# Kernel optimization log

Measured on AMD Instinct MI355X. Metric: run time of the kernel, lower is better.

The kernel has to match this reference:

```python
import jax, jax.numpy as jnp
import numpy as np

EPS = 1e-5

def conv1x1_bn(x, W, b, gamma, beta, mean, var):
    # x: (B,C,H,W); W: (O,C) 1x1 conv; BN in eval mode with running stats
    y = jnp.einsum('bchw,oc->bohw', x, W) + b[None, :, None, None]
    scale = gamma / jnp.sqrt(var + EPS)
    return y * scale[None, :, None, None] + (beta - mean * scale)[None, :, None, None]

def setup_inputs() -> dict:
    key = jax.random.key(0)
    ks = jax.random.split(key, 12)
    B, C, H, W = 8, 64, 128, 256
    d = {
        'fea_left': jax.random.normal(ks[0], (B, C, H, W), jnp.float32),
        'fea_right': jax.random.normal(ks[1], (B, C, H, W), jnp.float32),
        'Wq': jax.random.normal(ks[2], (C, C), jnp.float32) * (1.0 / np.sqrt(C)),
        'bq': jax.random.normal(ks[3], (C,), jnp.float32) * 0.02,
        'gq': 1.0 + 0.1 * jax.random.normal(ks[4], (C,), jnp.float32),
        'betaq': 0.02 * jax.random.normal(ks[5], (C,), jnp.float32),
        'mq': 0.02 * jax.random.normal(ks[6], (C,), jnp.float32),
        'vq': jax.random.uniform(ks[7], (C,), jnp.float32, 0.5, 1.5),
        'Wk': jax.random.normal(ks[8], (C, C), jnp.float32) * (1.0 / np.sqrt(C)),
        'bk': jax.random.normal(ks[9], (C,), jnp.float32) * 0.02,
        'gk': 1.0 + 0.1 * jax.random.normal(ks[10], (C,), jnp.float32),
        'betak': 0.02 * jax.random.normal(ks[11], (C,), jnp.float32),
        'mk': 0.02 * jax.random.normal(jax.random.fold_in(key, 100), (C,), jnp.float32),
        'vk': jax.random.uniform(jax.random.fold_in(key, 101), (C,), jnp.float32, 0.5, 1.5),
    }
    return d

def _attend(src, tgt, Wq, bq, gq, betaq, mq, vq, Wk, bk, gk, betak, mk, vk):
    # query from src, key from tgt, values are raw tgt features
    c = src.shape[1]
    Q = conv1x1_bn(src, Wq, bq, gq, betaq, mq, vq)   # (B,C,H,W)
    K = conv1x1_bn(tgt, Wk, bk, gk, betak, mk, vk)   # (B,C,H,W)
    # cost: (B,H,Wq,Wk) = Q^T K over channels, per image row
    cost = jnp.einsum('bchw,bchv->bhwv', Q, K) / c
    attn = jax.nn.softmax(cost, axis=-1)
    out = jnp.einsum('bhwv,bchv->bchw', attn, tgt)   # back to (B,C,H,W)
    return out

def reference(fea_left, fea_right, Wq, bq, gq, betaq, mq, vq, Wk, bk, gk, betak, mk, vk):
    cxr = _attend(fea_left, fea_right, Wq, bq, gq, betaq, mq, vq, Wk, bk, gk, betak, mk, vk)
    enh = _attend(fea_right, fea_left, Wq, bq, gq, betaq, mq, vq, Wk, bk, gk, betak, mk, vk)
    return (cxr, enh)
```

## Files before the change

### kernel.cpp

```cpp
#include <hip/hip_runtime.h>

#define HW_ 32768
#define OUTHALF 16777216ULL
#define SMEM_BYTES 117760

typedef short short8  __attribute__((ext_vector_type(8)));
typedef short short4v __attribute__((ext_vector_type(4)));
typedef float f32x4   __attribute__((ext_vector_type(4)));

__device__ __forceinline__ unsigned short f2bf(float f) {
  unsigned u = __builtin_bit_cast(unsigned, f);
  u += 0x7fffu + ((u >> 16) & 1u);
  return (unsigned short)(u >> 16);
}
__device__ __forceinline__ float bf2f(short s) {
  unsigned u = ((unsigned)(unsigned short)s) << 16;
  return __builtin_bit_cast(float, u);
}
__device__ __forceinline__ char* swz(char* base, int row, int colByte) {
  return base + row * 128 + (colByte ^ ((row & 7) << 4));
}
__device__ __forceinline__ f32x4 zero4() { f32x4 z = {0.f, 0.f, 0.f, 0.f}; return z; }

__global__ void pam_setup(const float* __restrict__ Wq, const float* __restrict__ bq,
                          const float* __restrict__ gq, const float* __restrict__ betaq,
                          const float* __restrict__ mq, const float* __restrict__ vq,
                          const float* __restrict__ Wk, const float* __restrict__ gk,
                          const float* __restrict__ vk,
                          short* __restrict__ Mb, float* __restrict__ u) {
  int blk = blockIdx.x, tid = threadIdx.x;
  if (blk < 16) {
    int entry = blk * 256 + tid;
    int x = entry >> 6, y = entry & 63;
    float acc = 0.f;
    for (int o = 0; o < 64; ++o) {
      float sq = gq[o] * rsqrtf(vq[o] + 1e-5f);
      float sk = gk[o] * rsqrtf(vk[o] + 1e-5f);
      acc += Wq[o * 64 + x] * sq * Wk[o * 64 + y] * sk;
    }
    Mb[x * 64 + y] = (short)f2bf(acc);
  } else if (tid < 64) {
    int y = tid;
    float acc = 0.f;
    for (int o = 0; o < 64; ++o) {
      float sq = gq[o] * rsqrtf(vq[o] + 1e-5f);
      float sk = gk[o] * rsqrtf(vk[o] + 1e-5f);
      float bqq = bq[o] * sq + betaq[o] - mq[o] * sq;
      acc += bqq * Wk[o * 64 + y] * sk;
    }
    u[y] = acc;
  }
}

__global__ __launch_bounds__(512, 2) void pam_main(
    const float* __restrict__ fl, const float* __restrict__ fr,
    const short* __restrict__ Mb, const float* __restrict__ uvec,
    float* __restrict__ out) {
  extern __shared__ __align__(16) char sm[];
  char* XLt = sm;
  char* XRt = sm + 32768;
  char* Kt  = sm + 65536;
  char* Xn  = sm + 73728;
  char* Pt  = sm + 81920;
  float* tl = (float*)(sm + 114688);
  float* Db = (float*)(sm + 116736);

  const int tid  = threadIdx.x;
  const int lane = tid & 63;
  const int wave = tid >> 6;
  const int l15  = lane & 15;
  const int g    = lane >> 4;
  const int bb   = blockIdx.x >> 7;
  const int hh   = blockIdx.x & 127;
  const int rowOff = hh * 256;
  const int base_b = bb * 64;

  for (int it = 0; it < 16; ++it) {
    int unit = it * 512 + tid;
    int tensor = unit >> 12;
    int rem = unit & 4095;
    int cq = rem >> 8;
    int p  = rem & 255;
    const float* src = tensor ? fr : fl;
    char* dst = tensor ? XRt : XLt;
    int gbase = (base_b + cq * 4) * HW_ + rowOff + p;
    float v0 = src[gbase];
    float v1 = src[gbase + HW_];
    float v2 = src[gbase + 2 * HW_];
    float v3 = src[gbase + 3 * HW_];
    short4v pk;
    pk[0] = (short)f2bf(v0); pk[1] = (short)f2bf(v1);
    pk[2] = (short)f2bf(v2); pk[3] = (short)f2bf(v3);
    *(short4v*)swz(dst, p, cq * 8) = pk;
  }
  __syncthreads();

  {
    int sel = tid >> 8;
    int p   = tid & 255;
    char* xt = sel ? XLt : XRt;
    float acc = 0.f;
    #pragma unroll
    for (int j = 0; j < 8; ++j) {
      short8 xv = *(const short8*)swz(xt, p, j * 16);
      #pragma unroll
      for (int e = 0; e < 8; ++e)
        acc = fmaf(bf2f(xv[e]), uvec[j * 8 + e], acc);
    }
    tl[sel * 256 + p] = acc * 0.015625f;
  }

  const short8* mbv = (const short8*)Mb;

  for (int at = 0; at < 2; ++at) {
    char* Xq  = at ? XRt : XLt;
    char* Xkv = at ? XLt : XRt;
    const float* skv = at ? fl : fr;
    const float* tp  = tl + at * 256;
    float* outp = out + (at ? OUTHALF : 0) + (size_t)base_b * HW_ + rowOff;

    f32x4 acc_o[2][4];
    #pragma unroll
    for (int i = 0; i < 2; ++i)
      #pragma unroll
      for (int j = 0; j < 4; ++j) acc_o[i][j] = zero4();
    float dacc0 = 0.f, dacc1 = 0.f;
    const int w0 = wave * 32;

    for (int vt = 0; vt < 4; ++vt) {
      __syncthreads();
      {
        int c  = tid >> 3;
        int v8 = (tid & 7) * 8;
        const float* s = skv + (base_b + c) * HW_ + rowOff + vt * 64 + v8;
        f32x4 A0 = *(const f32x4*)s;
        f32x4 A1 = *(const f32x4*)(s + 4);
        short8 pk;
        pk[0] = (short)f2bf(A0[0]); pk[1] = (short)f2bf(A0[1]);
        pk[2] = (short)f2bf(A0[2]); pk[3] = (short)f2bf(A0[3]);
        pk[4] = (short)f2bf(A1[0]); pk[5] = (short)f2bf(A1[1]);
        pk[6] = (short)f2bf(A1[2]); pk[7] = (short)f2bf(A1[3]);
        *(short8*)swz(Xn, c, v8 * 2) = pk;
      }
      #pragma unroll
      for (int s2 = 0; s2 < 2; ++s2) {
        int sidx = wave * 2 + s2;
        int mi = sidx >> 2, nj = sidx & 3;
        f32x4 accc = zero4();
        #pragma unroll
        for (int kk = 0; kk < 2; ++kk) {
          short8 af = *(const short8*)swz(Xkv, vt * 64 + mi * 16 + l15, (kk * 32 + 8 * g) * 2);
          short8 bf = mbv[(nj * 16 + l15) * 8 + kk * 4 + g];
          accc = __builtin_amdgcn_mfma_f32_16x16x32_bf16(af, bf, accc, 0, 0, 0);
        }
        int e2 = (nj * 16 + l15) * 2;
        #pragma unroll
        for (int r = 0; r < 4; ++r)
          *(short*)swz(Kt, mi * 16 + 4 * g + r, e2) = (short)f2bf(accc[r]);
      }
      __syncthreads();

      short8 bqf[2][2];
      #pragma unroll
      for (int nj = 0; nj < 2; ++nj)
        #pragma unroll
        for (int kk = 0; kk < 2; ++kk)
          bqf[nj][kk] = *(const short8*)swz(Xq, w0 + nj * 16 + l15, (kk * 32 + 8 * g) * 2);

      f32x4 accs[4][2];
      #pragma unroll
      for (int mi = 0; mi < 4; ++mi) {
        accs[mi][0] = zero4(); accs[mi][1] = zero4();
        #pragma unroll
        for (int kk = 0; kk < 2; ++kk) {
          short8 af = *(const short8*)swz(Kt, mi * 16 + l15, (kk * 32 + 8 * g) * 2);
          accs[mi][0] = __builtin_amdgcn_mfma_f32_16x16x32_bf16(af, bqf[0][kk], accs[mi][0], 0, 0, 0);
          accs[mi][1] = __builtin_amdgcn_mfma_f32_16x16x32_bf16(af, bqf[1][kk], accs[mi][1], 0, 0, 0);
        }
      }
      #pragma unroll
      for (int mi = 0; mi < 4; ++mi) {
        f32x4 tr = *(const f32x4*)(tp + vt * 64 + mi * 16 + 4 * g);
        #pragma unroll
        for (int nj = 0; nj < 2; ++nj) {
          f32x4 pv;
          #pragma unroll
          for (int r = 0; r < 4; ++r)
            pv[r] = __expf(fmaf(accs[mi][nj][r], 0.015625f, tr[r]));
          if (nj == 0) dacc0 += pv[0] + pv[1] + pv[2] + pv[3];
          else         dacc1 += pv[0] + pv[1] + pv[2] + pv[3];
          short4v p4;
          p4[0] = (short)f2bf(pv[0]); p4[1] = (short)f2bf(pv[1]);
          p4[2] = (short)f2bf(pv[2]); p4[3] = (short)f2bf(pv[3]);
          *(short4v*)swz(Pt, wave * 32 + nj * 16 + l15, mi * 32 + 8 * g) = p4;
        }
      }
      #pragma unroll
      for (int kk = 0; kk < 2; ++kk) {
        short8 pa0 = *(const short8*)swz(Pt, wave * 32 + l15,      (kk * 32 + 8 * g) * 2);
        short8 pa1 = *(const short8*)swz(Pt, wave * 32 + 16 + l15, (kk * 32 + 8 * g) * 2);
        #pragma unroll
        for (int nj2 = 0; nj2 < 4; ++nj2) {
          short8 xb = *(const short8*)swz(Xn, nj2 * 16 + l15, (kk * 32 + 8 * g) * 2);
          acc_o[0][nj2] = __builtin_amdgcn_mfma_f32_16x16x32_bf16(pa0, xb, acc_o[0][nj2], 0, 0, 0);
          acc_o[1][nj2] = __builtin_amdgcn_mfma_f32_16x16x32_bf16(pa1, xb, acc_o[1][nj2], 0, 0, 0);
        }
      }
    }

    dacc0 += __shfl_xor(dacc0, 16); dacc0 += __shfl_xor(dacc0, 32);
    dacc1 += __shfl_xor(dacc1, 16); dacc1 += __shfl_xor(dacc1, 32);
    if (lane < 16) {
      Db[wave * 32 + lane]      = __builtin_amdgcn_rcpf(dacc0);
      Db[wave * 32 + 16 + lane] = __builtin_amdgcn_rcpf(dacc1);
    }
    #pragma unroll
    for (int mi2 = 0; mi2 < 2; ++mi2) {
      f32x4 rd = *(const f32x4*)(Db + wave * 32 + mi2 * 16 + 4 * g);
      #pragma unroll
      for (int nj2 = 0; nj2 < 4; ++nj2) {
        int c = nj2 * 16 + l15;
        f32x4 v;
        v[0] = acc_o[mi2][nj2][0] * rd[0];
        v[1] = acc_o[mi2][nj2][1] * rd[1];
        v[2] = acc_o[mi2][nj2][2] * rd[2];
        v[3] = acc_o[mi2][nj2][3] * rd[3];
        *(f32x4*)(outp + (size_t)c * HW_ + w0 + mi2 * 16 + 4 * g) = v;
      }
    }
  }
}

extern "C" void kernel_launch(void* const* d_in, const int* in_sizes, int n_in,
                              void* d_out, int out_size, void* d_ws, size_t ws_size,
                              hipStream_t stream) {
  (void)in_sizes; (void)n_in; (void)out_size; (void)ws_size;
  const float* fl    = (const float*)d_in[0];
  const float* fr    = (const float*)d_in[1];
  const float* Wq    = (const float*)d_in[2];
  const float* bq    = (const float*)d_in[3];
  const float* gq    = (const float*)d_in[4];
  const float* betaq = (const float*)d_in[5];
  const float* mq    = (const float*)d_in[6];
  const float* vq    = (const float*)d_in[7];
  const float* Wk    = (const float*)d_in[8];
  const float* gk    = (const float*)d_in[10];
  const float* vk    = (const float*)d_in[13];
  short* Mb = (short*)d_ws;
  float* u  = (float*)((char*)d_ws + 8192);
  float* out = (float*)d_out;

  hipFuncSetAttribute((const void*)pam_main,
                      hipFuncAttributeMaxDynamicSharedMemorySize, SMEM_BYTES);
  pam_setup<<<17, 256, 0, stream>>>(Wq, bq, gq, betaq, mq, vq, Wk, gk, vk, Mb, u);
  pam_main<<<1024, 512, SMEM_BYTES, stream>>>(fl, fr, Mb, u, out);
}
```

Before: 127.3 us.

## Split attention directions across blocks and shrink LDS for higher occupancy

Each block now handles a single attention direction (left→right or right→left) instead of both, which doubles the grid and drops the second transposed tile from shared memory. LDS per block falls from about 115 KB to 66 KB, and launch bounds now allow 4 blocks per CU. Query fragments are loaded straight from global memory into registers, the next value tile is prefetched into registers while the current one is being computed, and the P tile is handled one 16-row half at a time to cut register pressure. In exchange, each row's key/value data is reloaded and reconverted by two blocks, and the strided per-element query loads from global memory may coalesce poorly.

```diff
diff --git a/kernel.cpp b/kernel.cpp
--- a/kernel.cpp
+++ b/kernel.cpp
@@ -2,7 +2,7 @@
 
 #define HW_ 32768
 #define OUTHALF 16777216ULL
-#define SMEM_BYTES 117760
+#define SMEM_BYTES 67584
 
 typedef short short8  __attribute__((ext_vector_type(8)));
 typedef short short4v __attribute__((ext_vector_type(4)));
@@ -52,181 +52,180 @@
   }
 }
 
-__global__ __launch_bounds__(512, 2) void pam_main(
+__global__ __launch_bounds__(512, 4) void pam_main(
     const float* __restrict__ fl, const float* __restrict__ fr,
     const short* __restrict__ Mb, const float* __restrict__ uvec,
     float* __restrict__ out) {
   extern __shared__ __align__(16) char sm[];
-  char* XLt = sm;
-  char* XRt = sm + 32768;
-  char* Kt  = sm + 65536;
-  char* Xn  = sm + 73728;
-  char* Pt  = sm + 81920;
-  float* tl = (float*)(sm + 114688);
-  float* Db = (float*)(sm + 116736);
+  char* Xt = sm;
+  char* Kt = sm + 32768;
+  char* Xn = sm + 40960;
+  char* Pt = sm + 49152;
+  float* tl = (float*)(sm + 65536);
+  float* Db = (float*)(sm + 66560);
 
   const int tid  = threadIdx.x;
   const int lane = tid & 63;
   const int wave = tid >> 6;
   const int l15  = lane & 15;
   const int g    = lane >> 4;
-  const int bb   = blockIdx.x >> 7;
-  const int hh   = blockIdx.x & 127;
+  const int bh   = blockIdx.x >> 1;
+  const int at   = blockIdx.x & 1;
+  const int bb   = bh >> 7;
+  const int hh   = bh & 127;
   const int rowOff = hh * 256;
   const int base_b = bb * 64;
-
-  for (int it = 0; it < 16; ++it) {
+  const int w0   = wave * 32;
+
+  const float* srcq  = at ? fr : fl;
+  const float* srckv = at ? fl : fr;
+  float* outp = out + (at ? OUTHALF : 0) + (size_t)base_b * HW_ + rowOff;
+
+  short8 bqf[2][2];
+  #pragma unroll
+  for (int nj = 0; nj < 2; ++nj) {
+    #pragma unroll
+    for (int kk = 0; kk < 2; ++kk) {
+      const float* qp = srcq + (size_t)(base_b + kk * 32 + 8 * g) * HW_
+                      + rowOff + w0 + nj * 16 + l15;
+      short8 q;
+      #pragma unroll
+      for (int e = 0; e < 8; ++e) q[e] = (short)f2bf(qp[(size_t)e * HW_]);
+      bqf[nj][kk] = q;
+    }
+  }
+
+  #pragma unroll
+  for (int it = 0; it < 8; ++it) {
     int unit = it * 512 + tid;
-    int tensor = unit >> 12;
-    int rem = unit & 4095;
-    int cq = rem >> 8;
-    int p  = rem & 255;
-    const float* src = tensor ? fr : fl;
-    char* dst = tensor ? XRt : XLt;
-    int gbase = (base_b + cq * 4) * HW_ + rowOff + p;
-    float v0 = src[gbase];
-    float v1 = src[gbase + HW_];
-    float v2 = src[gbase + 2 * HW_];
-    float v3 = src[gbase + 3 * HW_];
+    int cq = unit >> 8;
+    int p  = unit & 255;
+    const float* s = srckv + (size_t)(base_b + cq * 4) * HW_ + rowOff + p;
+    float v0 = s[0];
+    float v1 = s[HW_];
+    float v2 = s[2 * HW_];
+    float v3 = s[3 * HW_];
     short4v pk;
     pk[0] = (short)f2bf(v0); pk[1] = (short)f2bf(v1);
     pk[2] = (short)f2bf(v2); pk[3] = (short)f2bf(v3);
-    *(short4v*)swz(dst, p, cq * 8) = pk;
+    *(short4v*)swz(Xt, p, cq * 8) = pk;
   }
   __syncthreads();
 
-  {
-    int sel = tid >> 8;
-    int p   = tid & 255;
-    char* xt = sel ? XLt : XRt;
+  if (tid < 256) {
     float acc = 0.f;
     #pragma unroll
     for (int j = 0; j < 8; ++j) {
-      short8 xv = *(const short8*)swz(xt, p, j * 16);
+      short8 xv = *(const short8*)swz(Xt, tid, j * 16);
       #pragma unroll
       for (int e = 0; e < 8; ++e)
         acc = fmaf(bf2f(xv[e]), uvec[j * 8 + e], acc);
     }
-    tl[sel * 256 + p] = acc * 0.015625f;
+    tl[tid] = acc * 0.015625f;
   }
 
   const short8* mbv = (const short8*)Mb;
-
-  for (int at = 0; at < 2; ++at) {
-    char* Xq  = at ? XRt : XLt;
-    char* Xkv = at ? XLt : XRt;
-    const float* skv = at ? fl : fr;
-    const float* tp  = tl + at * 256;
-    float* outp = out + (at ? OUTHALF : 0) + (size_t)base_b * HW_ + rowOff;
-
-    f32x4 acc_o[2][4];
-    #pragma unroll
-    for (int i = 0; i < 2; ++i)
-      #pragma unroll
-      for (int j = 0; j < 4; ++j) acc_o[i][j] = zero4();
-    float dacc0 = 0.f, dacc1 = 0.f;
-    const int w0 = wave * 32;
-
-    for (int vt = 0; vt < 4; ++vt) {
-      __syncthreads();
-      {
-        int c  = tid >> 3;
-        int v8 = (tid & 7) * 8;
-        const float* s = skv + (base_b + c) * HW_ + rowOff + vt * 64 + v8;
-        f32x4 A0 = *(const f32x4*)s;
-        f32x4 A1 = *(const f32x4*)(s + 4);
-        short8 pk;
-        pk[0] = (short)f2bf(A0[0]); pk[1] = (short)f2bf(A0[1]);
-        pk[2] = (short)f2bf(A0[2]); pk[3] = (short)f2bf(A0[3]);
-        pk[4] = (short)f2bf(A1[0]); pk[5] = (short)f2bf(A1[1]);
-        pk[6] = (short)f2bf(A1[2]); pk[7] = (short)f2bf(A1[3]);
-        *(short8*)swz(Xn, c, v8 * 2) = pk;
+  char* Ptw = Pt + wave * 2048;
+
+  f32x4 acc_o[2][4];
+  #pragma unroll
+  for (int i = 0; i < 2; ++i)
+    #pragma unroll
+    for (int j = 0; j < 4; ++j) acc_o[i][j] = zero4();
+  float dacc0 = 0.f, dacc1 = 0.f;
+
+  const int vc = tid >> 3;
+  const int v8 = (tid & 7) * 8;
+  const float* vbase = srckv + (size_t)(base_b + vc) * HW_ + rowOff + v8;
+  f32x4 A0 = *(const f32x4*)(vbase);
+  f32x4 A1 = *(const f32x4*)(vbase + 4);
+
+  for (int vt = 0; vt < 4; ++vt) {
+    if (vt) __syncthreads();
+    {
+      short8 pk;
+      pk[0] = (short)f2bf(A0[0]); pk[1] = (short)f2bf(A0[1]);
+      pk[2] = (short)f2bf(A0[2]); pk[3] = (short)f2bf(A0[3]);
+      pk[4] = (short)f2bf(A1[0]); pk[5] = (short)f2bf(A1[1]);
+      pk[6] = (short)f2bf(A1[2]); pk[7] = (short)f2bf(A1[3]);
+      *(short8*)swz(Xn, vc, v8 * 2) = pk;
+    }
+    #pragma unroll
+    for (int s2 = 0; s2 < 2; ++s2) {
+      int sidx = wave * 2 + s2;
+      int mi = sidx >> 2, njc = sidx & 3;
+      f32x4 accc = zero4();
+      #pragma unroll
+      for (int kk = 0; kk < 2; ++kk) {
+        short8 af = *(const short8*)swz(Xt, vt * 64 + mi * 16 + l15, (kk * 32 + 8 * g) * 2);
+        short8 bf = mbv[(njc * 16 + l15) * 8 + kk * 4 + g];
+        accc = __builtin_amdgcn_mfma_f32_16x16x32_bf16(af, bf, accc, 0, 0, 0);
       }
-      #pragma unroll
-      for (int s2 = 0; s2 < 2; ++s2) {
-        int sidx = wave * 2 + s2;
-        int mi = sidx >> 2, nj = sidx & 3;
-        f32x4 accc = zero4();
-        #pragma unroll
-        for (int kk = 0; kk < 2; ++kk) {
-          short8 af = *(const short8*)swz(Xkv, vt * 64 + mi * 16 + l15, (kk * 32 + 8 * g) * 2);
-          short8 bf = mbv[(nj * 16 + l15) * 8 + kk * 4 + g];
-          accc = __builtin_amdgcn_mfma_f32_16x16x32_bf16(af, bf, accc, 0, 0, 0);
-        }
-        int e2 = (nj * 16 + l15) * 2;
-        #pragma unroll
-        for (int r = 0; r < 4; ++r)
-          *(short*)swz(Kt, mi * 16 + 4 * g + r, e2) = (short)f2bf(accc[r]);
-      }
-      __syncthreads();
-
-      short8 bqf[2][2];
-      #pragma unroll
-      for (int nj = 0; nj < 2; ++nj)
-        #pragma unroll
-        for (int kk = 0; kk < 2; ++kk)
-          bqf[nj][kk] = *(const short8*)swz(Xq, w0 + nj * 16 + l15, (kk * 32 + 8 * g) * 2);
-
-      f32x4 accs[4][2];
+      int e2 = (njc * 16 + l15) * 2;
+      #pragma unroll
+      for (int r = 0; r < 4; ++r)
+        *(short*)swz(Kt, mi * 16 + 4 * g + r, e2) = (short)f2bf(accc[r]);
+    }
+    __syncthreads();
+
+    if (vt < 3) {
+      A0 = *(const f32x4*)(vbase + (vt + 1) * 64);
+      A1 = *(const f32x4*)(vbase + (vt + 1) * 64 + 4);
+    }
+
+    #pragma unroll
+    for (int nj = 0; nj < 2; ++nj) {
+      float dloc = 0.f;
       #pragma unroll
       for (int mi = 0; mi < 4; ++mi) {
-        accs[mi][0] = zero4(); accs[mi][1] = zero4();
+        f32x4 a = zero4();
         #pragma unroll
         for (int kk = 0; kk < 2; ++kk) {
           short8 af = *(const short8*)swz(Kt, mi * 16 + l15, (kk * 32 + 8 * g) * 2);
-          accs[mi][0] = __builtin_amdgcn_mfma_f32_16x16x32_bf16(af, bqf[0][kk], accs[mi][0], 0, 0, 0);
-          accs[mi][1] = __builtin_amdgcn_mfma_f32_16x16x32_bf16(af, bqf[1][kk], accs[mi][1], 0, 0, 0);
+          a = __builtin_amdgcn_mfma_f32_16x16x32_bf16(af, bqf[nj][kk], a, 0, 0, 0);
         }
+        f32x4 tr = *(const f32x4*)(tl + vt * 64 + mi * 16 + 4 * g);
+        f32x4 pv;
+        #pragma unroll
+        for (int r = 0; r < 4; ++r)
+          pv[r] = __expf(fmaf(a[r], 0.015625f, tr[r]));
+        dloc += pv[0] + pv[1] + pv[2] + pv[3];
+        short4v p4;
+        p4[0] = (short)f2bf(pv[0]); p4[1] = (short)f2bf(pv[1]);
+        p4[2] = (short)f2bf(pv[2]); p4[3] = (short)f2bf(pv[3]);
+        *(short4v*)swz(Ptw, l15, mi * 32 + 8 * g) = p4;
       }
-      #pragma unroll
-      for (int mi = 0; mi < 4; ++mi) {
-        f32x4 tr = *(const f32x4*)(tp + vt * 64 + mi * 16 + 4 * g);
-        #pragma unroll
-        for (int nj = 0; nj < 2; ++nj) {
-          f32x4 pv;
-          #pragma unroll
-          for (int r = 0; r < 4; ++r)
-            pv[r] = __expf(fmaf(accs[mi][nj][r], 0.015625f, tr[r]));
-          if (nj == 0) dacc0 += pv[0] + pv[1] + pv[2] + pv[3];
-          else         dacc1 += pv[0] + pv[1] + pv[2] + pv[3];
-          short4v p4;
-          p4[0] = (short)f2bf(pv[0]); p4[1] = (short)f2bf(pv[1]);
-          p4[2] = (short)f2bf(pv[2]); p4[3] = (short)f2bf(pv[3]);
-          *(short4v*)swz(Pt, wave * 32 + nj * 16 + l15, mi * 32 + 8 * g) = p4;
-        }
-      }
+      if (nj == 0) dacc0 += dloc; else dacc1 += dloc;
       #pragma unroll
       for (int kk = 0; kk < 2; ++kk) {
-        short8 pa0 = *(const short8*)swz(Pt, wave * 32 + l15,      (kk * 32 + 8 * g) * 2);
-        short8 pa1 = *(const short8*)swz(Pt, wave * 32 + 16 + l15, (kk * 32 + 8 * g) * 2);
+        short8 pa = *(const short8*)swz(Ptw, l15, kk * 64 + 16 * g);
         #pragma unroll
         for (int nj2 = 0; nj2 < 4; ++nj2) {
           short8 xb = *(const short8*)swz(Xn, nj2 * 16 + l15, (kk * 32 + 8 * g) * 2);
-          acc_o[0][nj2] = __builtin_amdgcn_mfma_f32_16x16x32_bf16(pa0, xb, acc_o[0][nj2], 0, 0, 0);
-          acc_o[1][nj2] = __builtin_amdgcn_mfma_f32_16x16x32_bf16(pa1, xb, acc_o[1][nj2], 0, 0, 0);
+          acc_o[nj][nj2] = __builtin_amdgcn_mfma_f32_16x16x32_bf16(pa, xb, acc_o[nj][nj2], 0, 0, 0);
         }
       }
     }
-
-    dacc0 += __shfl_xor(dacc0, 16); dacc0 += __shfl_xor(dacc0, 32);
-    dacc1 += __shfl_xor(dacc1, 16); dacc1 += __shfl_xor(dacc1, 32);
-    if (lane < 16) {
-      Db[wave * 32 + lane]      = __builtin_amdgcn_rcpf(dacc0);
-      Db[wave * 32 + 16 + lane] = __builtin_amdgcn_rcpf(dacc1);
-    }
-    #pragma unroll
-    for (int mi2 = 0; mi2 < 2; ++mi2) {
-      f32x4 rd = *(const f32x4*)(Db + wave * 32 + mi2 * 16 + 4 * g);
-      #pragma unroll
-      for (int nj2 = 0; nj2 < 4; ++nj2) {
-        int c = nj2 * 16 + l15;
-        f32x4 v;
-        v[0] = acc_o[mi2][nj2][0] * rd[0];
-        v[1] = acc_o[mi2][nj2][1] * rd[1];
-        v[2] = acc_o[mi2][nj2][2] * rd[2];
-        v[3] = acc_o[mi2][nj2][3] * rd[3];
-        *(f32x4*)(outp + (size_t)c * HW_ + w0 + mi2 * 16 + 4 * g) = v;
-      }
+  }
+
+  dacc0 += __shfl_xor(dacc0, 16); dacc0 += __shfl_xor(dacc0, 32);
+  dacc1 += __shfl_xor(dacc1, 16); dacc1 += __shfl_xor(dacc1, 32);
+  if (lane < 16) {
+    Db[wave * 32 + lane]      = __builtin_amdgcn_rcpf(dacc0);
+    Db[wave * 32 + 16 + lane] = __builtin_amdgcn_rcpf(dacc1);
+  }
+  #pragma unroll
+  for (int mi2 = 0; mi2 < 2; ++mi2) {
+    f32x4 rd = *(const f32x4*)(Db + wave * 32 + mi2 * 16 + 4 * g);
+    #pragma unroll
+    for (int nj2 = 0; nj2 < 4; ++nj2) {
+      int c = nj2 * 16 + l15;
+      f32x4 v;
+      v[0] = acc_o[mi2][nj2][0] * rd[0];
+      v[1] = acc_o[mi2][nj2][1] * rd[1];
+      v[2] = acc_o[mi2][nj2][2] * rd[2];
+      v[3] = acc_o[mi2][nj2][3] * rd[3];
+      *(f32x4*)(outp + (size_t)c * HW_ + w0 + mi2 * 16 + 4 * g) = v;
     }
   }
 }
@@ -253,5 +252,5 @@
   hipFuncSetAttribute((const void*)pam_main,
                       hipFuncAttributeMaxDynamicSharedMemorySize, SMEM_BYTES);
   pam_setup<<<17, 256, 0, stream>>>(Wq, bq, gq, betaq, mq, vq, Wk, gk, vk, Mb, u);
-  pam_main<<<1024, 512, SMEM_BYTES, stream>>>(fl, fr, Mb, u, out);
-}
+  pam_main<<<2048, 512, SMEM_BYTES, stream>>>(fl, fr, Mb, u, out);
+}
```

Result: slower. 164.6 us (+29.3%).

## Project queries through M once per wave and double-buffer value tiles with 1024 threads

Applied to the files above, without the earlier changes.

The blocks grow to 1024 threads, so each of 16 waves owns 16 query columns. Each wave computes its projected query (M^T x_q) once per direction and keeps it in registers, instead of projecting every key tile through M on each iteration. The value tile loads are double-buffered in shared memory with a register prefetch, which leaves one barrier per tile. The risks are register pressure from the launch_bounds(1024,4) request and the occupancy limit set by the roughly 115 KB of shared memory per block.

```diff
diff --git a/kernel.cpp b/kernel.cpp
--- a/kernel.cpp
+++ b/kernel.cpp
@@ -27,18 +27,18 @@
                           const float* __restrict__ mq, const float* __restrict__ vq,
                           const float* __restrict__ Wk, const float* __restrict__ gk,
                           const float* __restrict__ vk,
-                          short* __restrict__ Mb, float* __restrict__ u) {
+                          short* __restrict__ Mbt, float* __restrict__ u) {
   int blk = blockIdx.x, tid = threadIdx.x;
   if (blk < 16) {
     int entry = blk * 256 + tid;
-    int x = entry >> 6, y = entry & 63;
+    int y = entry >> 6, x = entry & 63;
     float acc = 0.f;
     for (int o = 0; o < 64; ++o) {
       float sq = gq[o] * rsqrtf(vq[o] + 1e-5f);
       float sk = gk[o] * rsqrtf(vk[o] + 1e-5f);
       acc += Wq[o * 64 + x] * sq * Wk[o * 64 + y] * sk;
     }
-    Mb[x * 64 + y] = (short)f2bf(acc);
+    Mbt[y * 64 + x] = (short)f2bf(acc);
   } else if (tid < 64) {
     int y = tid;
     float acc = 0.f;
@@ -52,15 +52,14 @@
   }
 }
 
-__global__ __launch_bounds__(512, 2) void pam_main(
+__global__ __launch_bounds__(1024, 4) void pam_main(
     const float* __restrict__ fl, const float* __restrict__ fr,
-    const short* __restrict__ Mb, const float* __restrict__ uvec,
+    const short* __restrict__ Mbt, const float* __restrict__ uvec,
     float* __restrict__ out) {
   extern __shared__ __align__(16) char sm[];
   char* XLt = sm;
   char* XRt = sm + 32768;
-  char* Kt  = sm + 65536;
-  char* Xn  = sm + 73728;
+  char* Xn0 = sm + 65536;
   char* Pt  = sm + 81920;
   float* tl = (float*)(sm + 114688);
   float* Db = (float*)(sm + 116736);
@@ -74,30 +73,28 @@
   const int hh   = blockIdx.x & 127;
   const int rowOff = hh * 256;
   const int base_b = bb * 64;
-
-  for (int it = 0; it < 16; ++it) {
-    int unit = it * 512 + tid;
+  const int w0   = wave * 16;
+
+  char* Ptw = Pt + wave * 2048;
+
+  #pragma unroll
+  for (int it = 0; it < 8; ++it) {
+    int unit = it * 1024 + tid;
     int tensor = unit >> 12;
     int rem = unit & 4095;
     int cq = rem >> 8;
     int p  = rem & 255;
-    const float* src = tensor ? fr : fl;
-    char* dst = tensor ? XRt : XLt;
-    int gbase = (base_b + cq * 4) * HW_ + rowOff + p;
-    float v0 = src[gbase];
-    float v1 = src[gbase + HW_];
-    float v2 = src[gbase + 2 * HW_];
-    float v3 = src[gbase + 3 * HW_];
+    const float* s = (tensor ? fr : fl) + (size_t)(base_b + cq * 4) * HW_ + rowOff + p;
+    float v0 = s[0], v1 = s[HW_], v2 = s[2 * HW_], v3 = s[3 * HW_];
     short4v pk;
     pk[0] = (short)f2bf(v0); pk[1] = (short)f2bf(v1);
     pk[2] = (short)f2bf(v2); pk[3] = (short)f2bf(v3);
-    *(short4v*)swz(dst, p, cq * 8) = pk;
+    *(short4v*)swz(tensor ? XRt : XLt, p, cq * 8) = pk;
   }
   __syncthreads();
 
-  {
-    int sel = tid >> 8;
-    int p   = tid & 255;
+  if (tid < 512) {
+    int sel = tid >> 8, p = tid & 255;
     char* xt = sel ? XLt : XRt;
     float acc = 0.f;
     #pragma unroll
@@ -110,8 +107,7 @@
     tl[sel * 256 + p] = acc * 0.015625f;
   }
 
-  const short8* mbv = (const short8*)Mb;
-
+  #pragma unroll 1
   for (int at = 0; at < 2; ++at) {
     char* Xq  = at ? XRt : XLt;
     char* Xkv = at ? XLt : XRt;
@@ -119,114 +115,106 @@
     const float* tp  = tl + at * 256;
     float* outp = out + (at ? OUTHALF : 0) + (size_t)base_b * HW_ + rowOff;
 
-    f32x4 acc_o[2][4];
+    short8 bq_[2];
+    {
+      short8 xb_[2];
+      #pragma unroll
+      for (int kk = 0; kk < 2; ++kk)
+        xb_[kk] = *(const short8*)swz(Xq, w0 + l15, (kk * 32 + 8 * g) * 2);
+      #pragma unroll
+      for (int mi = 0; mi < 4; ++mi) {
+        f32x4 q = zero4();
+        #pragma unroll
+        for (int kk = 0; kk < 2; ++kk) {
+          short8 am = *(const short8*)(Mbt + (mi * 16 + l15) * 64 + kk * 32 + 8 * g);
+          q = __builtin_amdgcn_mfma_f32_16x16x32_bf16(am, xb_[kk], q, 0, 0, 0);
+        }
+        short4v p4;
+        p4[0] = (short)f2bf(q[0]); p4[1] = (short)f2bf(q[1]);
+        p4[2] = (short)f2bf(q[2]); p4[3] = (short)f2bf(q[3]);
+        *(short4v*)swz(Ptw, l15, mi * 32 + 8 * g) = p4;
+      }
+      #pragma unroll
+      for (int kk = 0; kk < 2; ++kk)
+        bq_[kk] = *(const short8*)swz(Ptw, l15, kk * 64 + 16 * g);
+    }
+
+    f32x4 acc_o[4];
     #pragma unroll
-    for (int i = 0; i < 2; ++i)
-      #pragma unroll
-      for (int j = 0; j < 4; ++j) acc_o[i][j] = zero4();
-    float dacc0 = 0.f, dacc1 = 0.f;
-    const int w0 = wave * 32;
+    for (int j = 0; j < 4; ++j) acc_o[j] = zero4();
+    float dacc = 0.f;
+
+    const int vc = tid >> 4;
+    const int v4 = (tid & 15) * 4;
+    const float* vbase = skv + (size_t)(base_b + vc) * HW_ + rowOff + v4;
+    f32x4 A0 = *(const f32x4*)vbase;
+    {
+      short4v pk;
+      pk[0] = (short)f2bf(A0[0]); pk[1] = (short)f2bf(A0[1]);
+      pk[2] = (short)f2bf(A0[2]); pk[3] = (short)f2bf(A0[3]);
+      *(short4v*)swz(Xn0, vc, v4 * 2) = pk;
+    }
+    A0 = *(const f32x4*)(vbase + 64);
+    __syncthreads();
 
     for (int vt = 0; vt < 4; ++vt) {
-      __syncthreads();
-      {
-        int c  = tid >> 3;
-        int v8 = (tid & 7) * 8;
-        const float* s = skv + (base_b + c) * HW_ + rowOff + vt * 64 + v8;
-        f32x4 A0 = *(const f32x4*)s;
-        f32x4 A1 = *(const f32x4*)(s + 4);
-        short8 pk;
+      if (vt < 3) {
+        short4v pk;
         pk[0] = (short)f2bf(A0[0]); pk[1] = (short)f2bf(A0[1]);
         pk[2] = (short)f2bf(A0[2]); pk[3] = (short)f2bf(A0[3]);
-        pk[4] = (short)f2bf(A1[0]); pk[5] = (short)f2bf(A1[1]);
-        pk[6] = (short)f2bf(A1[2]); pk[7] = (short)f2bf(A1[3]);
-        *(short8*)swz(Xn, c, v8 * 2) = pk;
-      }
-      #pragma unroll
-      for (int s2 = 0; s2 < 2; ++s2) {
-        int sidx = wave * 2 + s2;
-        int mi = sidx >> 2, nj = sidx & 3;
-        f32x4 accc = zero4();
+        *(short4v*)swz(Xn0 + ((vt + 1) & 1) * 8192, vc, v4 * 2) = pk;
+      }
+      if (vt < 2) A0 = *(const f32x4*)(vbase + (vt + 2) * 64);
+      char* XnB = Xn0 + (vt & 1) * 8192;
+
+      f32x4 accs[4];
+      #pragma unroll
+      for (int mi = 0; mi < 4; ++mi) {
+        accs[mi] = zero4();
         #pragma unroll
         for (int kk = 0; kk < 2; ++kk) {
-          short8 af = *(const short8*)swz(Xkv, vt * 64 + mi * 16 + l15, (kk * 32 + 8 * g) * 2);
-          short8 bf = mbv[(nj * 16 + l15) * 8 + kk * 4 + g];
-          accc = __builtin_amdgcn_mfma_f32_16x16x32_bf16(af, bf, accc, 0, 0, 0);
-        }
-        int e2 = (nj * 16 + l15) * 2;
-        #pragma unroll
-        for (int r = 0; r < 4; ++r)
-          *(short*)swz(Kt, mi * 16 + 4 * g + r, e2) = (short)f2bf(accc[r]);
-      }
-      __syncthreads();
-
-      short8 bqf[2][2];
-      #pragma unroll
-      for (int nj = 0; nj < 2; ++nj)
-        #pragma unroll
-        for (int kk = 0; kk < 2; ++kk)
-          bqf[nj][kk] = *(const short8*)swz(Xq, w0 + nj * 16 + l15, (kk * 32 + 8 * g) * 2);
-
-      f32x4 accs[4][2];
-      #pragma unroll
-      for (int mi = 0; mi < 4; ++mi) {
-        accs[mi][0] = zero4(); accs[mi][1] = zero4();
-        #pragma unroll
-        for (int kk = 0; kk < 2; ++kk) {
-          short8 af = *(const short8*)swz(Kt, mi * 16 + l15, (kk * 32 + 8 * g) * 2);
-          accs[mi][0] = __builtin_amdgcn_mfma_f32_16x16x32_bf16(af, bqf[0][kk], accs[mi][0], 0, 0, 0);
-          accs[mi][1] = __builtin_amdgcn_mfma_f32_16x16x32_bf16(af, bqf[1][kk], accs[mi][1], 0, 0, 0);
+          short8 af = *(const short8*)swz(Xkv, vt * 64 + mi * 16 + l15,
+                                          (kk * 32 + 8 * g) * 2);
+          accs[mi] = __builtin_amdgcn_mfma_f32_16x16x32_bf16(af, bq_[kk], accs[mi], 0, 0, 0);
         }
       }
       #pragma unroll
       for (int mi = 0; mi < 4; ++mi) {
         f32x4 tr = *(const f32x4*)(tp + vt * 64 + mi * 16 + 4 * g);
-        #pragma unroll
-        for (int nj = 0; nj < 2; ++nj) {
-          f32x4 pv;
-          #pragma unroll
-          for (int r = 0; r < 4; ++r)
-            pv[r] = __expf(fmaf(accs[mi][nj][r], 0.015625f, tr[r]));
-          if (nj == 0) dacc0 += pv[0] + pv[1] + pv[2] + pv[3];
-          else         dacc1 += pv[0] + pv[1] + pv[2] + pv[3];
-          short4v p4;
-          p4[0] = (short)f2bf(pv[0]); p4[1] = (short)f2bf(pv[1]);
-          p4[2] = (short)f2bf(pv[2]); p4[3] = (short)f2bf(pv[3]);
-          *(short4v*)swz(Pt, wave * 32 + nj * 16 + l15, mi * 32 + 8 * g) = p4;
+        f32x4 pv;
+        #pragma unroll
+        for (int r = 0; r < 4; ++r)
+          pv[r] = __expf(fmaf(accs[mi][r], 0.015625f, tr[r]));
+        dacc += pv[0] + pv[1] + pv[2] + pv[3];
+        short4v p4;
+        p4[0] = (short)f2bf(pv[0]); p4[1] = (short)f2bf(pv[1]);
+        p4[2] = (short)f2bf(pv[2]); p4[3] = (short)f2bf(pv[3]);
+        *(short4v*)swz(Ptw, l15, mi * 32 + 8 * g) = p4;
+      }
+      #pragma unroll
+      for (int kk = 0; kk < 2; ++kk) {
+        short8 pa = *(const short8*)swz(Ptw, l15, kk * 64 + 16 * g);
+        #pragma unroll
+        for (int nj2 = 0; nj2 < 4; ++nj2) {
+          short8 xb = *(const short8*)swz(XnB, nj2 * 16 + l15, (kk * 32 + 8 * g) * 2);
+          acc_o[nj2] = __builtin_amdgcn_mfma_f32_16x16x32_bf16(pa, xb, acc_o[nj2], 0, 0, 0);
         }
       }
-      #pragma unroll
-      for (int kk = 0; kk < 2; ++kk) {
-        short8 pa0 = *(const short8*)swz(Pt, wave * 32 + l15,      (kk * 32 + 8 * g) * 2);
-        short8 pa1 = *(const short8*)swz(Pt, wave * 32 + 16 + l15, (kk * 32 + 8 * g) * 2);
-        #pragma unroll
-        for (int nj2 = 0; nj2 < 4; ++nj2) {
-          short8 xb = *(const short8*)swz(Xn, nj2 * 16 + l15, (kk * 32 + 8 * g) * 2);
-          acc_o[0][nj2] = __builtin_amdgcn_mfma_f32_16x16x32_bf16(pa0, xb, acc_o[0][nj2], 0, 0, 0);
-          acc_o[1][nj2] = __builtin_amdgcn_mfma_f32_16x16x32_bf16(pa1, xb, acc_o[1][nj2], 0, 0, 0);
-        }
-      }
-    }
-
-    dacc0 += __shfl_xor(dacc0, 16); dacc0 += __shfl_xor(dacc0, 32);
-    dacc1 += __shfl_xor(dacc1, 16); dacc1 += __shfl_xor(dacc1, 32);
-    if (lane < 16) {
-      Db[wave * 32 + lane]      = __builtin_amdgcn_rcpf(dacc0);
-      Db[wave * 32 + 16 + lane] = __builtin_amdgcn_rcpf(dacc1);
-    }
+      __syncthreads();
+    }
+
+    dacc += __shfl_xor(dacc, 16); dacc += __shfl_xor(dacc, 32);
+    if (lane < 16) Db[wave * 16 + lane] = __builtin_amdgcn_rcpf(dacc);
+    f32x4 rd = *(const f32x4*)(Db + wave * 16 + 4 * g);
     #pragma unroll
-    for (int mi2 = 0; mi2 < 2; ++mi2) {
-      f32x4 rd = *(const f32x4*)(Db + wave * 32 + mi2 * 16 + 4 * g);
-      #pragma unroll
-      for (int nj2 = 0; nj2 < 4; ++nj2) {
-        int c = nj2 * 16 + l15;
-        f32x4 v;
-        v[0] = acc_o[mi2][nj2][0] * rd[0];
-        v[1] = acc_o[mi2][nj2][1] * rd[1];
-        v[2] = acc_o[mi2][nj2][2] * rd[2];
-        v[3] = acc_o[mi2][nj2][3] * rd[3];
-        *(f32x4*)(outp + (size_t)c * HW_ + w0 + mi2 * 16 + 4 * g) = v;
-      }
+    for (int nj2 = 0; nj2 < 4; ++nj2) {
+      int c = nj2 * 16 + l15;
+      f32x4 v;
+      v[0] = acc_o[nj2][0] * rd[0];
+      v[1] = acc_o[nj2][1] * rd[1];
+      v[2] = acc_o[nj2][2] * rd[2];
+      v[3] = acc_o[nj2][3] * rd[3];
+      *(f32x4*)(outp + (size_t)c * HW_ + w0 + 4 * g) = v;
     }
   }
 }
@@ -246,12 +234,12 @@
   const float* Wk    = (const float*)d_in[8];
   const float* gk    = (const float*)d_in[10];
   const float* vk    = (const float*)d_in[13];
-  short* Mb = (short*)d_ws;
-  float* u  = (float*)((char*)d_ws + 8192);
+  short* Mbt = (short*)d_ws;
+  float* u   = (float*)((char*)d_ws + 8192);
   float* out = (float*)d_out;
 
   hipFuncSetAttribute((const void*)pam_main,
                       hipFuncAttributeMaxDynamicSharedMemorySize, SMEM_BYTES);
-  pam_setup<<<17, 256, 0, stream>>>(Wq, bq, gq, betaq, mq, vq, Wk, gk, vk, Mb, u);
-  pam_main<<<1024, 512, SMEM_BYTES, stream>>>(fl, fr, Mb, u, out);
-}
+  pam_setup<<<17, 256, 0, stream>>>(Wq, bq, gq, betaq, mq, vq, Wk, gk, vk, Mbt, u);
+  pam_main<<<1024, 1024, SMEM_BYTES, stream>>>(fl, fr, Mbt, u, out);
+}
```

Result: no change. 127.7 us (+0.3%).
